# Optimization experiments

Hardware: AMD Instinct MI355X
Metric: run time of the kernel (lower is better)

## Reference

```python
import jax, jax.numpy as jnp
import numpy as np
from jax import lax

BOUNDARY_PER_ITERATION = [3, 2, 1, 0]  # boundary_width=4, boundary_iteration=4


def _cross_dilate(x):
    # grayscale dilation with 3x3 cross structuring element (max over center+4-neighbors)
    p = jnp.pad(x, ((0, 0), (0, 0), (1, 1), (1, 1)), constant_values=-jnp.inf)
    c = p[:, :, 1:-1, 1:-1]
    up = p[:, :, :-2, 1:-1]
    dn = p[:, :, 2:, 1:-1]
    lf = p[:, :, 1:-1, :-2]
    rt = p[:, :, 1:-1, 2:]
    return jnp.maximum(jnp.maximum(jnp.maximum(c, up), jnp.maximum(dn, lf)), rt)


def _full_erode(x):
    # grayscale erosion with full 3x3 structuring element (min over 3x3 window)
    return lax.reduce_window(x, jnp.inf, lax.min, (1, 1, 3, 3), (1, 1, 1, 1),
                             ((0, 0), (0, 0), (1, 1), (1, 1)))


def _box3_sum(x):
    # conv2d with all-ones 3x3 kernel, padding='same'
    return lax.reduce_window(x, 0.0, lax.add, (1, 1, 3, 3), (1, 1, 1, 1),
                             ((0, 0), (0, 0), (1, 1), (1, 1)))


def _find_boundaries(pred_f):
    return (_cross_dilate(pred_f) != _full_erode(pred_f)).astype(pred_f.dtype)


def _expand_boundaries(b, r):
    # dilation with diamond of radius r == r applications of cross dilation
    for _ in range(r):
        b = _cross_dilate(b)
    return b


def _gaussian_kernel_2d(n, std):
    i = np.arange(n, dtype=np.float64) - (n - 1) / 2.0
    g = np.exp(-(i ** 2) / (2.0 * std ** 2))
    g /= g.sum()
    return np.outer(g, g).astype(np.float32)  # cv2.getGaussianKernel outer product


def setup_inputs() -> dict:
    key = jax.random.key(0)
    k1, k2, k3 = jax.random.split(key, 3)
    n, c, h, w = 8, 19, 512, 512
    x = jax.random.normal(k1, (n, c, h, w), dtype=jnp.float32)
    means = jax.random.normal(k2, (c,), dtype=jnp.float32)
    std = jax.random.uniform(k3, (c,), dtype=jnp.float32) + 0.5  # positive variances
    gaussian_kernel = jnp.asarray(_gaussian_kernel_2d(7, 1.0))[None, None]  # (1,1,7,7)
    return {"x": x, "means": means, "std": std, "gaussian_kernel": gaussian_kernel}


def reference(x, means, std, gaussian_kernel):
    # max logits and prediction
    max_logits = jnp.max(x, axis=1, keepdims=True)           # (n,1,h,w)
    pred = jnp.argmax(x, axis=1, keepdims=True)              # (n,1,h,w) int
    sml = (max_logits - means[pred]) / std[pred]             # standardized max logits

    # boundary suppression
    pred_f = pred.astype(sml.dtype)
    boundaries = _find_boundaries(pred_f)
    for r in BOUNDARY_PER_ITERATION:
        expanded = _expand_boundaries(boundaries, r)
        nb_mask = (expanded == 0).astype(sml.dtype)
        sml_masked = sml * nb_mask
        sml_nb = _box3_sum(sml_masked)
        nb_cnt = _box3_sum(nb_mask)
        sml_avg = jnp.where(nb_cnt == 0, sml, sml_nb / jnp.where(nb_cnt == 0, 1.0, nb_cnt))
        sml = jnp.where(nb_mask == 0, sml_avg, sml)

    # dilated smoothing (gaussian conv, padding same)
    sml = lax.conv_general_dilated(sml, gaussian_kernel, (1, 1), 'SAME',
                                   dimension_numbers=('NCHW', 'OIHW', 'NCHW'))
    return sml, pred
```

## Files before the change

kernel.cpp:

```cpp
#include <hip/hip_runtime.h>
#include <cstdint>
#include <cstddef>

#define W_ 512
#define H_ 512
#define N_ 8
#define C_ 19
#define HW_ (W_*H_)
#define NPIX_ (N_*HW_)

#define TS  32
#define SR  46
#define SC  48
#define BR  52

typedef float   f32x4 __attribute__((ext_vector_type(4)));
typedef float   f32x2 __attribute__((ext_vector_type(2)));
typedef uint8_t u8x2  __attribute__((ext_vector_type(2)));
typedef unsigned long long u64;

__global__ __launch_bounds__(256) void k_argmax_sml(
    const float* __restrict__ x, const float* __restrict__ means,
    const float* __restrict__ stdv, float* __restrict__ sml,
    uint8_t* __restrict__ pred8, float* __restrict__ predf)
{
    __shared__ float xs[C_ * 512];
    __shared__ float ms[C_], rs[C_];
    const int tid = threadIdx.x;
    if (tid < C_) {
        ms[tid] = means[tid];
        rs[tid] = __builtin_amdgcn_rcpf(stdv[tid]);
    }

    const int chunk = blockIdx.x;
    const int n   = chunk >> 9;
    const int p0  = (chunk & 511) << 9;
    const int wv  = tid >> 6, lane = tid & 63;
    const float* xg = x + (size_t)n * C_ * HW_ + p0;

    int cLo = wv * 5;
    int cHi = cLo + 5 > C_ ? C_ : cLo + 5;
    for (int c = cLo; c < cHi; ++c) {
        const float* g = xg + (size_t)c * HW_ + lane * 4;
        #pragma unroll
        for (int t = 0; t < 2; ++t) {
            __builtin_amdgcn_global_load_lds(
                (const __attribute__((address_space(1))) void*)(g + t * 256),
                (__attribute__((address_space(3))) void*)&xs[c * 512 + t * 256],
                16, 0, 0);
        }
    }
    __syncthreads();

    const f32x2* xv = (const f32x2*)xs;
    f32x2 mv = xv[tid];
    int i0 = 0, i1 = 0;
    #pragma unroll
    for (int c = 1; c < C_; ++c) {
        f32x2 v = xv[c * 256 + tid];
        if (v[0] > mv[0]) { mv[0] = v[0]; i0 = c; }
        if (v[1] > mv[1]) { mv[1] = v[1]; i1 = c; }
    }
    const int pix = chunk * 512 + tid * 2;
    f32x2 s, pf; u8x2 pc;
    s[0] = (mv[0] - ms[i0]) * rs[i0];  pf[0] = (float)i0;  pc[0] = (uint8_t)i0;
    s[1] = (mv[1] - ms[i1]) * rs[i1];  pf[1] = (float)i1;  pc[1] = (uint8_t)i1;
    *(f32x2*)(sml + pix) = s;
    *(u8x2*)(pred8 + pix) = pc;
    __builtin_nontemporal_store(pf, (f32x2*)(predf + pix));
}

__global__ __launch_bounds__(256) void k_bnd(
    const uint8_t* __restrict__ pred8, u64* __restrict__ bndM)
{
    int gid  = blockIdx.x * 256 + threadIdx.x;
    int lane = gid & 63;
    int wave = gid >> 6;
    int w = wave & 7;
    int y = (wave >> 3) & 511;
    int n = wave >> 12;
    int xx = w * 64 + lane;
    const uint8_t* pc = pred8 + (size_t)n * HW_ + y * W_ + xx;
    int c = pc[0];
    bool u = y > 0, d = y < H_-1, l = xx > 0, r = xx < W_-1;
    int up = u ? pc[-W_] : c;
    int dn = d ? pc[ W_] : c;
    int lf = l ? pc[-1]  : c;
    int rt = r ? pc[ 1]  : c;
    int mx = max(max(c, up), max(dn, max(lf, rt)));
    int mn = min(min(c, up), min(dn, min(lf, rt)));
    int c00 = (u && l) ? pc[-W_-1] : c;
    int c01 = (u && r) ? pc[-W_+1] : c;
    int c10 = (d && l) ? pc[ W_-1] : c;
    int c11 = (d && r) ? pc[ W_+1] : c;
    mn = min(mn, min(min(c00, c01), min(c10, c11)));
    u64 m = __ballot(mx != mn);
    if (lane == 0) bndM[((size_t)n * 512 + y) * 8 + w] = m;
}

__global__ __launch_bounds__(256) void k_fused(
    const float* __restrict__ sml_g, const u64* __restrict__ bndM,
    const float* __restrict__ gk, float* __restrict__ out)
{
    __shared__ float smlA[SR*SC];
    __shared__ float smlB[SR*SC];
    __shared__ u64 M0[BR], E1[BR], E2[BR], E3[BR], VM[BR];
    __shared__ u64 NBM[4][BR];
    __shared__ float g7[7];
    __shared__ int tACT;

    const int tid = threadIdx.x;
    const int bx = blockIdx.x, by = blockIdx.y, n = blockIdx.z;
    const int tx0 = bx * TS, ty0 = by * TS;
    const float* sg = sml_g + (size_t)n * HW_;

    if (tid == 0) tACT = 0;
    if (tid < 7) g7[tid] = gk[21 + tid] / sqrtf(gk[24]);

    if (tid < BR) {
        int gy = ty0 + tid - 10;
        int bx0 = tx0 - 10;
        u64 m = 0, vm = 0;
        if (gy >= 0 && gy < H_) {
            const u64* row = bndM + ((size_t)n * 512 + gy) * 8;
            int sft = bx0 & 63;
            int wi  = bx0 >> 6;
            u64 w0 = (wi >= 0) ? row[wi] : 0ULL;
            u64 w1 = (wi + 1 <= 7) ? row[wi + 1] : 0ULL;
            m = sft ? ((w0 >> sft) | (w1 << (64 - sft))) : w0;
            int lo = bx0 < 0 ? -bx0 : 0;
            int hi = (512 - bx0) < BR ? (512 - bx0) : BR;
            if (hi > lo) vm = ((1ULL << (hi - lo)) - 1ULL) << lo;
        }
        M0[tid] = m;
        VM[tid] = vm;
    }
    __syncthreads();

    u64 actRow = 0;
    if (tid < SR) {
        int bi = tid + 3;
        u64 nbU = ~M0[bi-1] & VM[bi-1];
        u64 nbC = ~M0[bi  ] & VM[bi  ];
        u64 nbD = ~M0[bi+1] & VM[bi+1];
        u64 U = nbU | nbC | nbD;
        u64 A = (U >> 1) | (U >> 2) | (U >> 3);
        int lo = tx0 == 0 ? 8 : 0;
        int hi = tx0 == (W_-TS) ? 40 : SC;
        u64 CV = (hi - lo >= 64) ? ~0ULL : (((1ULL << (hi - lo)) - 1ULL) << lo);
        actRow = A & CV;
        int gy = ty0 + tid - 7;
        if ((unsigned)gy >= (unsigned)H_) actRow = 0;
        if (actRow) tACT = 1;
    }
    __syncthreads();

    if (!tACT) {
        for (int s = tid; s < 38 * 10; s += 256) {
            int q  = s / 10;
            int ly = 4 + q, lx4 = s - q * 10;
            int gy = ty0 + ly - 7;
            int gx = tx0 - 4 + lx4 * 4;
            f32x4 v = {0.f, 0.f, 0.f, 0.f};
            if ((unsigned)gy < (unsigned)H_ && (unsigned)gx < (unsigned)W_)
                v = *(const f32x4*)(sg + (size_t)gy * W_ + gx);
            *(f32x4*)&smlA[ly * SC + 4 + lx4 * 4] = v;
        }
        __syncthreads();
        float* htmp = smlB;
        for (int s = tid; s < 38 * 32; s += 256) {
            int hy = s >> 5, hx = s & 31;
            const float* p = &smlA[(hy + 4)*SC + (hx + 5)];
            htmp[hy*33 + hx] = g7[0]*p[0] + g7[1]*p[1] + g7[2]*p[2] + g7[3]*p[3]
                             + g7[4]*p[4] + g7[5]*p[5] + g7[6]*p[6];
        }
        __syncthreads();
        for (int s = tid; s < TS*TS; s += 256) {
            int oy = s >> 5, ox = s & 31;
            const float* p = &htmp[oy*33 + ox];
            float a = g7[0]*p[0]   + g7[1]*p[33]  + g7[2]*p[66]  + g7[3]*p[99]
                    + g7[4]*p[132] + g7[5]*p[165] + g7[6]*p[198];
            out[(size_t)n*HW_ + (size_t)(ty0 + oy)*W_ + (tx0 + ox)] = a;
        }
        return;
    }

    if (bx > 0 && bx < (W_/TS - 1)) {
        for (int s = tid; s < SR * (SC/4); s += 256) {
            int ly = s / (SC/4), j = s - ly * (SC/4);
            int gy = ty0 + ly - 7;
            f32x4 v = {0.f, 0.f, 0.f, 0.f};
            if ((unsigned)gy < (unsigned)H_)
                v = *(const f32x4*)(sg + (size_t)gy * W_ + (tx0 - 8) + j * 4);
            *(f32x4*)&smlA[ly * SC + j * 4] = v;
        }
    } else {
        for (int s = tid; s < SR * SC; s += 256) {
            int ly = s / SC, lx = s - ly * SC;
            int gy = ty0 + ly - 7, gx = tx0 + lx - 8;
            float v = 0.f;
            if ((unsigned)gy < (unsigned)H_ && (unsigned)gx < (unsigned)W_)
                v = sg[(size_t)gy * W_ + gx];
            smlA[ly * SC + lx] = v;
        }
    }
    __syncthreads();

    if (tid < BR) {
        u64 a = M0[tid], u = tid > 0 ? M0[tid-1] : 0, d = tid < BR-1 ? M0[tid+1] : 0;
        E1[tid] = a | (a << 1) | (a >> 1) | u | d;
    }
    __syncthreads();
    if (tid < BR) {
        u64 a = E1[tid], u = tid > 0 ? E1[tid-1] : 0, d = tid < BR-1 ? E1[tid+1] : 0;
        E2[tid] = a | (a << 1) | (a >> 1) | u | d;
    }
    __syncthreads();
    if (tid < BR) {
        u64 a = E2[tid], u = tid > 0 ? E2[tid-1] : 0, d = tid < BR-1 ? E2[tid+1] : 0;
        E3[tid] = a | (a << 1) | (a >> 1) | u | d;
    }
    __syncthreads();
    {
        int r = tid >> 6, i = tid & 63;
        if (i < BR) {
            u64 e = (r == 0) ? M0[i] : (r == 1) ? E1[i] : (r == 2) ? E2[i] : E3[i];
            NBM[r][i] = ~e & VM[i];
        }
    }
    __syncthreads();

    #pragma unroll
    for (int k = 0; k < 4; ++k) {
        const int r = 3 - k;
        const u64 colmask = ((1ULL << (44 - 2*k)) - 1ULL) << (2 + k);
        u64 mwork = 0;
        if (tid >= 1 + k && tid < 45 - k && tid < SR)
            mwork = actRow & colmask;
        u64 mm = mwork;
        while (mm) {
            int lx = __ffsll(mm) - 1; mm &= mm - 1;
            int bi = tid + 3, sh = lx + 1;
            u64 fu = (NBM[r][bi-1] >> sh) & 7ULL;
            u64 fc = (NBM[r][bi  ] >> sh) & 7ULL;
            u64 fd = (NBM[r][bi+1] >> sh) & 7ULL;
            float c = smlA[tid*SC + lx];
            float o;
            if (((fc >> 1) & 1ULL) || !(fu | fc | fd)) {
                o = c;
            } else {
                int cnt = __popcll(fu) + __popcll(fc) + __popcll(fd);
                float sum = 0.f;
                const float* r0 = &smlA[(tid-1)*SC + lx];
                const float* r1 = &smlA[(tid  )*SC + lx];
                const float* r2 = &smlA[(tid+1)*SC + lx];
                if (fu & 1) sum += r0[-1];
                if (fu & 2) sum += r0[0];
                if (fu & 4) sum += r0[1];
                if (fc & 1) sum += r1[-1];
                if (fc & 4) sum += r1[1];
                if (fd & 1) sum += r2[-1];
                if (fd & 2) sum += r2[0];
                if (fd & 4) sum += r2[1];
                o = sum / (float)cnt;
            }
            smlB[tid*SC + lx] = o;
        }
        __syncthreads();
        mm = mwork;
        while (mm) {
            int lx = __ffsll(mm) - 1; mm &= mm - 1;
            smlA[tid*SC + lx] = smlB[tid*SC + lx];
        }
        __syncthreads();
    }

    float* htmp = smlB;
    for (int s = tid; s < 38 * 32; s += 256) {
        int hy = s >> 5, hx = s & 31;
        const float* p = &smlA[(hy + 4)*SC + (hx + 5)];
        htmp[hy*33 + hx] = g7[0]*p[0] + g7[1]*p[1] + g7[2]*p[2] + g7[3]*p[3]
                         + g7[4]*p[4] + g7[5]*p[5] + g7[6]*p[6];
    }
    __syncthreads();
    for (int s = tid; s < TS*TS; s += 256) {
        int oy = s >> 5, ox = s & 31;
        const float* p = &htmp[oy*33 + ox];
        float a = g7[0]*p[0]   + g7[1]*p[33]  + g7[2]*p[66]  + g7[3]*p[99]
                + g7[4]*p[132] + g7[5]*p[165] + g7[6]*p[198];
        out[(size_t)n*HW_ + (size_t)(ty0 + oy)*W_ + (tx0 + ox)] = a;
    }
}

extern "C" void kernel_launch(void* const* d_in, const int* in_sizes, int n_in,
                              void* d_out, int out_size, void* d_ws, size_t ws_size,
                              hipStream_t stream)
{
    const float* x     = (const float*)d_in[0];
    const float* means = (const float*)d_in[1];
    const float* stdv  = (const float*)d_in[2];
    const float* gk    = (const float*)d_in[3];
    float* out_sml  = (float*)d_out;
    float* out_pred = (float*)d_out + NPIX_;

    char* ws = (char*)d_ws;
    float*   sml   = (float*)(ws);
    uint8_t* pred8 = (uint8_t*)(ws + 8388608);
    u64*     bndM  = (u64*)(ws + 10485760);

    k_argmax_sml<<<NPIX_/512, 256, 0, stream>>>(x, means, stdv, sml, pred8, out_pred);
    k_bnd<<<NPIX_/256, 256, 0, stream>>>(pred8, bndM);
    dim3 fgrd(W_/TS, H_/TS, N_);
    k_fused<<<fgrd, 256, 0, stream>>>(sml, bndM, gk, out_sml);
}
```

Before: 51.34 us.

## Fuse boundary detection and pred float output into the tiled fused kernel

Removes the separate k_bnd launch. Each tile of k_fused now loads a clamped 54x54 patch of uint8 predictions into LDS and computes the boundary bitmasks there with ballots. The float pred output write also moves from the argmax kernel into the fused kernel, reusing the LDS patch. This saves one kernel launch, the bndM round trip through global memory and a store stream in the argmax kernel. In exchange the halo pred bytes are loaded redundantly per tile and extra LDS plus a synchronisation are added.

```diff
diff --git a/kernel.cpp b/kernel.cpp
--- a/kernel.cpp
+++ b/kernel.cpp
@@ -13,6 +13,7 @@
 #define SR  46
 #define SC  48
 #define BR  52
+#define PP  56
 
 typedef float   f32x4 __attribute__((ext_vector_type(4)));
 typedef float   f32x2 __attribute__((ext_vector_type(2)));
@@ -22,7 +23,7 @@
 __global__ __launch_bounds__(256) void k_argmax_sml(
     const float* __restrict__ x, const float* __restrict__ means,
     const float* __restrict__ stdv, float* __restrict__ sml,
-    uint8_t* __restrict__ pred8, float* __restrict__ predf)
+    uint8_t* __restrict__ pred8)
 {
     __shared__ float xs[C_ * 512];
     __shared__ float ms[C_], rs[C_];
@@ -62,46 +63,19 @@
         if (v[1] > mv[1]) { mv[1] = v[1]; i1 = c; }
     }
     const int pix = chunk * 512 + tid * 2;
-    f32x2 s, pf; u8x2 pc;
-    s[0] = (mv[0] - ms[i0]) * rs[i0];  pf[0] = (float)i0;  pc[0] = (uint8_t)i0;
-    s[1] = (mv[1] - ms[i1]) * rs[i1];  pf[1] = (float)i1;  pc[1] = (uint8_t)i1;
+    f32x2 s; u8x2 pc;
+    s[0] = (mv[0] - ms[i0]) * rs[i0];  pc[0] = (uint8_t)i0;
+    s[1] = (mv[1] - ms[i1]) * rs[i1];  pc[1] = (uint8_t)i1;
     *(f32x2*)(sml + pix) = s;
     *(u8x2*)(pred8 + pix) = pc;
-    __builtin_nontemporal_store(pf, (f32x2*)(predf + pix));
 }
 
-__global__ __launch_bounds__(256) void k_bnd(
-    const uint8_t* __restrict__ pred8, u64* __restrict__ bndM)
+__global__ __launch_bounds__(256) void k_fused(
+    const float* __restrict__ sml_g, const uint8_t* __restrict__ pred8,
+    const float* __restrict__ gk, float* __restrict__ out,
+    float* __restrict__ predf)
 {
-    int gid  = blockIdx.x * 256 + threadIdx.x;
-    int lane = gid & 63;
-    int wave = gid >> 6;
-    int w = wave & 7;
-    int y = (wave >> 3) & 511;
-    int n = wave >> 12;
-    int xx = w * 64 + lane;
-    const uint8_t* pc = pred8 + (size_t)n * HW_ + y * W_ + xx;
-    int c = pc[0];
-    bool u = y > 0, d = y < H_-1, l = xx > 0, r = xx < W_-1;
-    int up = u ? pc[-W_] : c;
-    int dn = d ? pc[ W_] : c;
-    int lf = l ? pc[-1]  : c;
-    int rt = r ? pc[ 1]  : c;
-    int mx = max(max(c, up), max(dn, max(lf, rt)));
-    int mn = min(min(c, up), min(dn, min(lf, rt)));
-    int c00 = (u && l) ? pc[-W_-1] : c;
-    int c01 = (u && r) ? pc[-W_+1] : c;
-    int c10 = (d && l) ? pc[ W_-1] : c;
-    int c11 = (d && r) ? pc[ W_+1] : c;
-    mn = min(mn, min(min(c00, c01), min(c10, c11)));
-    u64 m = __ballot(mx != mn);
-    if (lane == 0) bndM[((size_t)n * 512 + y) * 8 + w] = m;
-}
-
-__global__ __launch_bounds__(256) void k_fused(
-    const float* __restrict__ sml_g, const u64* __restrict__ bndM,
-    const float* __restrict__ gk, float* __restrict__ out)
-{
+    __shared__ uint8_t predT[54*PP];
     __shared__ float smlA[SR*SC];
     __shared__ float smlB[SR*SC];
     __shared__ u64 M0[BR], E1[BR], E2[BR], E3[BR], VM[BR];
@@ -110,32 +84,59 @@
     __shared__ int tACT;
 
     const int tid = threadIdx.x;
+    const int wv = tid >> 6, lane = tid & 63;
     const int bx = blockIdx.x, by = blockIdx.y, n = blockIdx.z;
     const int tx0 = bx * TS, ty0 = by * TS;
-    const float* sg = sml_g + (size_t)n * HW_;
+    const float*   sg = sml_g + (size_t)n * HW_;
+    const uint8_t* pg = pred8 + (size_t)n * HW_;
 
     if (tid == 0) tACT = 0;
     if (tid < 7) g7[tid] = gk[21 + tid] / sqrtf(gk[24]);
 
+    for (int s = tid; s < 54*54; s += 256) {
+        int i = s / 54, j = s - i * 54;
+        int gy = ty0 + i - 11; gy = gy < 0 ? 0 : (gy > H_-1 ? H_-1 : gy);
+        int gx = tx0 + j - 11; gx = gx < 0 ? 0 : (gx > W_-1 ? W_-1 : gx);
+        predT[i*PP + j] = pg[gy*W_ + gx];
+    }
     if (tid < BR) {
-        int gy = ty0 + tid - 10;
+        int gy  = ty0 + tid - 10;
         int bx0 = tx0 - 10;
-        u64 m = 0, vm = 0;
+        u64 vm = 0;
         if (gy >= 0 && gy < H_) {
-            const u64* row = bndM + ((size_t)n * 512 + gy) * 8;
-            int sft = bx0 & 63;
-            int wi  = bx0 >> 6;
-            u64 w0 = (wi >= 0) ? row[wi] : 0ULL;
-            u64 w1 = (wi + 1 <= 7) ? row[wi + 1] : 0ULL;
-            m = sft ? ((w0 >> sft) | (w1 << (64 - sft))) : w0;
             int lo = bx0 < 0 ? -bx0 : 0;
             int hi = (512 - bx0) < BR ? (512 - bx0) : BR;
             if (hi > lo) vm = ((1ULL << (hi - lo)) - 1ULL) << lo;
         }
-        M0[tid] = m;
         VM[tid] = vm;
     }
     __syncthreads();
+
+    for (int i = wv; i < BR; i += 4) {
+        bool b = false;
+        if (lane < BR) {
+            const uint8_t* p = &predT[(i+1)*PP + (lane+1)];
+            int c  = p[0];
+            int up = p[-PP], dn = p[PP], lf = p[-1], rt = p[1];
+            int mx = max(max(c, up), max(dn, max(lf, rt)));
+            int mn = min(min(c, up), min(dn, min(lf, rt)));
+            mn = min(mn, min(min((int)p[-PP-1], (int)p[-PP+1]),
+                             min((int)p[ PP-1], (int)p[ PP+1])));
+            b = (mx != mn);
+        }
+        u64 m = __ballot(b);
+        if (lane == 0) M0[i] = m & VM[i];
+    }
+    __syncthreads();
+
+    {
+        int oy = tid >> 3, ox4 = tid & 7;
+        f32x4 pf;
+        #pragma unroll
+        for (int k = 0; k < 4; ++k)
+            pf[k] = (float)predT[(oy + 11)*PP + (ox4*4 + k + 11)];
+        *(f32x4*)(predf + (size_t)n*HW_ + (size_t)(ty0 + oy)*W_ + tx0 + ox4*4) = pf;
+    }
 
     u64 actRow = 0;
     if (tid < SR) {
@@ -306,10 +307,8 @@
     char* ws = (char*)d_ws;
     float*   sml   = (float*)(ws);
     uint8_t* pred8 = (uint8_t*)(ws + 8388608);
-    u64*     bndM  = (u64*)(ws + 10485760);
-
-    k_argmax_sml<<<NPIX_/512, 256, 0, stream>>>(x, means, stdv, sml, pred8, out_pred);
-    k_bnd<<<NPIX_/256, 256, 0, stream>>>(pred8, bndM);
+
+    k_argmax_sml<<<NPIX_/512, 256, 0, stream>>>(x, means, stdv, sml, pred8);
     dim3 fgrd(W_/TS, H_/TS, N_);
-    k_fused<<<fgrd, 256, 0, stream>>>(sml, bndM, gk, out_sml);
+    k_fused<<<fgrd, 256, 0, stream>>>(sml, pred8, gk, out_sml, out_pred);
 }
```

After: 52.89 us. +3.0%, slower.

## Make argmax kernel persistent with double-buffered LDS prefetch of channel chunks

Applied to the files above, without the earlier changes.

The argmax/standardization kernel now launches 512 blocks, and each block processes 8 pixel chunks in a loop instead of one block per chunk. Two LDS buffers are used: the asynchronous global-to-LDS loads for the next chunk are issued before the current chunk is reduced. Hand-placed vmcnt waits and barriers make sure the current buffer has arrived. The aim is to hide the HBM load latency behind compute and cut block launch overhead. In exchange, LDS use per block doubles, which lowers the number of resident blocks per CU, and correctness now depends on the vmcnt counts matching the loads issued per wave.

```diff
diff --git a/kernel.cpp b/kernel.cpp
--- a/kernel.cpp
+++ b/kernel.cpp
@@ -24,50 +24,69 @@
     const float* __restrict__ stdv, float* __restrict__ sml,
     uint8_t* __restrict__ pred8, float* __restrict__ predf)
 {
-    __shared__ float xs[C_ * 512];
+    __shared__ float xs0[C_ * 512];
+    __shared__ float xs1[C_ * 512];
     __shared__ float ms[C_], rs[C_];
     const int tid = threadIdx.x;
     if (tid < C_) {
         ms[tid] = means[tid];
         rs[tid] = __builtin_amdgcn_rcpf(stdv[tid]);
     }
-
-    const int chunk = blockIdx.x;
-    const int n   = chunk >> 9;
-    const int p0  = (chunk & 511) << 9;
-    const int wv  = tid >> 6, lane = tid & 63;
-    const float* xg = x + (size_t)n * C_ * HW_ + p0;
-
-    int cLo = wv * 5;
-    int cHi = cLo + 5 > C_ ? C_ : cLo + 5;
-    for (int c = cLo; c < cHi; ++c) {
-        const float* g = xg + (size_t)c * HW_ + lane * 4;
+    const int wv = tid >> 6, lane = tid & 63;
+    const int cLo = wv * 5;
+    const int cHi = cLo + 5 > C_ ? C_ : cLo + 5;
+    const int bid = blockIdx.x;
+
+    auto issue = [&](int chunk, float* buf) {
+        const int n  = chunk >> 9;
+        const int p0 = (chunk & 511) << 9;
+        const float* xg = x + (size_t)n * C_ * HW_ + p0;
+        for (int c = cLo; c < cHi; ++c) {
+            const float* g = xg + (size_t)c * HW_ + lane * 4;
+            __builtin_amdgcn_global_load_lds(
+                (const __attribute__((address_space(1))) void*)g,
+                (__attribute__((address_space(3))) void*)&buf[c * 512], 16, 0, 0);
+            __builtin_amdgcn_global_load_lds(
+                (const __attribute__((address_space(1))) void*)(g + 256),
+                (__attribute__((address_space(3))) void*)&buf[c * 512 + 256], 16, 0, 0);
+        }
+    };
+
+    issue(bid, xs0);
+    #pragma unroll
+    for (int it = 0; it < 8; ++it) {
+        float* cur = (it & 1) ? xs1 : xs0;
+        float* nxt = (it & 1) ? xs0 : xs1;
+        if (it < 7) issue(bid + (it + 1) * 512, nxt);
+        __builtin_amdgcn_sched_barrier(0);
+        if (it < 7) {
+            if (wv < 3) asm volatile("s_waitcnt vmcnt(10)" ::: "memory");
+            else        asm volatile("s_waitcnt vmcnt(8)"  ::: "memory");
+        } else {
+            asm volatile("s_waitcnt vmcnt(0)" ::: "memory");
+        }
+        __builtin_amdgcn_s_barrier();
+        __builtin_amdgcn_sched_barrier(0);
+
+        const int chunk = bid + it * 512;
+        const f32x2* xv = (const f32x2*)cur;
+        f32x2 mv = xv[tid];
+        int i0 = 0, i1 = 0;
         #pragma unroll
-        for (int t = 0; t < 2; ++t) {
-            __builtin_amdgcn_global_load_lds(
-                (const __attribute__((address_space(1))) void*)(g + t * 256),
-                (__attribute__((address_space(3))) void*)&xs[c * 512 + t * 256],
-                16, 0, 0);
-        }
-    }
-    __syncthreads();
-
-    const f32x2* xv = (const f32x2*)xs;
-    f32x2 mv = xv[tid];
-    int i0 = 0, i1 = 0;
-    #pragma unroll
-    for (int c = 1; c < C_; ++c) {
-        f32x2 v = xv[c * 256 + tid];
-        if (v[0] > mv[0]) { mv[0] = v[0]; i0 = c; }
-        if (v[1] > mv[1]) { mv[1] = v[1]; i1 = c; }
-    }
-    const int pix = chunk * 512 + tid * 2;
-    f32x2 s, pf; u8x2 pc;
-    s[0] = (mv[0] - ms[i0]) * rs[i0];  pf[0] = (float)i0;  pc[0] = (uint8_t)i0;
-    s[1] = (mv[1] - ms[i1]) * rs[i1];  pf[1] = (float)i1;  pc[1] = (uint8_t)i1;
-    *(f32x2*)(sml + pix) = s;
-    *(u8x2*)(pred8 + pix) = pc;
-    __builtin_nontemporal_store(pf, (f32x2*)(predf + pix));
+        for (int c = 1; c < C_; ++c) {
+            f32x2 v = xv[c * 256 + tid];
+            if (v[0] > mv[0]) { mv[0] = v[0]; i0 = c; }
+            if (v[1] > mv[1]) { mv[1] = v[1]; i1 = c; }
+        }
+        const int pix = chunk * 512 + tid * 2;
+        f32x2 s, pf; u8x2 pc;
+        s[0] = (mv[0] - ms[i0]) * rs[i0];  pf[0] = (float)i0;  pc[0] = (uint8_t)i0;
+        s[1] = (mv[1] - ms[i1]) * rs[i1];  pf[1] = (float)i1;  pc[1] = (uint8_t)i1;
+        *(f32x2*)(sml + pix) = s;
+        *(u8x2*)(pred8 + pix) = pc;
+        __builtin_nontemporal_store(pf, (f32x2*)(predf + pix));
+        __builtin_amdgcn_s_barrier();
+    }
 }
 
 __global__ __launch_bounds__(256) void k_bnd(
@@ -308,7 +327,7 @@
     uint8_t* pred8 = (uint8_t*)(ws + 8388608);
     u64*     bndM  = (u64*)(ws + 10485760);
 
-    k_argmax_sml<<<NPIX_/512, 256, 0, stream>>>(x, means, stdv, sml, pred8, out_pred);
+    k_argmax_sml<<<512, 256, 0, stream>>>(x, means, stdv, sml, pred8, out_pred);
     k_bnd<<<NPIX_/256, 256, 0, stream>>>(pred8, bndM);
     dim3 fgrd(W_/TS, H_/TS, N_);
     k_fused<<<fgrd, 256, 0, stream>>>(sml, bndM, gk, out_sml);
```

New measurement: 52.16 us. No clear change (+1.6%).
